# Kernel optimization log

Hardware: AMD Instinct MI355X
Metric: run time of the kernel (lower is better)

## Reference

```python
import jax, jax.numpy as jnp
import numpy as np

# PGA G(3,0,1) basis order: [1, e0, e1, e2, e3, e01, e02, e03, e12, e13, e23, e012, e013, e023, e123, e0123].
# The invariant inner product <rev(x) y>_0 only involves blades NOT containing e0; for those blades
# the metric contribution is +1, so it is a plain dot product over these 8 components.
_IP_IDX = np.array([0, 2, 3, 4, 8, 9, 10, 14])
_EPS = 1e-3  # config.normalizer_eps


def _normalizer(x):
    # _lin_square_normalizer: x / (x^2 + eps), a bounded ~1/x-style transform
    return x / (x * x + _EPS)


def setup_inputs() -> dict:
    key = jax.random.key(0)
    ks = jax.random.split(key, 7)
    B, H, N, CMV, CS = 2, 8, 2048, 16, 32
    f = lambda k, s: jax.random.normal(k, s, dtype=jnp.float32)
    return {
        "q_mv": f(ks[0], (B, H, N, CMV, 16)),
        "k_mv": f(ks[1], (B, H, N, CMV, 16)),
        "v_mv": f(ks[2], (B, H, N, CMV, 16)),
        "q_s": f(ks[3], (B, H, N, CS)),
        "k_s": f(ks[4], (B, H, N, CS)),
        "v_s": f(ks[5], (B, H, N, CS)),
        "log_weights": 0.1 * f(ks[6], (H, 1, CMV)),
    }


def reference(q_mv, k_mv, v_mv, q_s, k_s, v_s, log_weights):
    B, H, N, CMV, _ = q_mv.shape
    CS = q_s.shape[-1]

    # per-head, per-mv-channel learned positive weights, broadcast over items and blades
    w = jnp.exp(log_weights)[None, :, :, :, None]  # (1, H, 1, CMV, 1)

    # Term 1: weighted PGA inner product of multivector q/k (8 non-degenerate blades per channel)
    q_ip = (q_mv[..., _IP_IDX] * w).reshape(B, H, N, CMV * 8)
    k_ip = k_mv[..., _IP_IDX].reshape(B, H, N, CMV * 8)

    # Term 2: transformed scalar inner product <phi(q_s), psi(k_s)> with phi=psi=normalizer
    # Term 3: Euclidean scalar inner product <q_s, k_s>
    q_feat = jnp.concatenate([q_ip, _normalizer(q_s), q_s], axis=-1)  # (B,H,N, 8*CMV + 2*CS)
    k_feat = jnp.concatenate([k_ip, _normalizer(k_s), k_s], axis=-1)

    scale = 1.0 / jnp.sqrt(jnp.asarray(q_feat.shape[-1], dtype=q_feat.dtype))
    scores = jnp.einsum("bhid,bhjd->bhij", q_feat, k_feat) * scale  # (B,H,N,N)
    attn = jax.nn.softmax(scores, axis=-1)

    # Shared attention weights applied to flattened multivector + scalar values
    v_flat = jnp.concatenate([v_mv.reshape(B, H, N, CMV * 16), v_s], axis=-1)  # (B,H,N, 16*CMV+CS)
    out = jnp.einsum("bhij,bhjd->bhid", attn, v_flat)

    out_mv = out[..., : CMV * 16].reshape(B, H, N, CMV, 16)
    out_s = out[..., CMV * 16 :]
    return out_mv, out_s
```

## Files before the change

### kernel.cpp

```cpp
#include <hip/hip_runtime.h>

typedef float f32x4 __attribute__((ext_vector_type(4)));
typedef _Float16 f16x8 __attribute__((ext_vector_type(8)));
typedef _Float16 f16x4 __attribute__((ext_vector_type(4)));

#define NSEQ 2048
#define KVBLK 64
#define NITER (NSEQ / KVBLK)
#define KFBYTES (KVBLK * 384)
#define VTBYTES (288 * 2 * KVBLK)
#define TILEB (KFBYTES + VTBYTES)
#define KFOFF 0
#define VTOFF KFBYTES
#define PSTRIDE 72
#define WS_NEED (16ull * NITER * TILEB)

#define SCALE_L2E 0.10411754f
#define DEFER_THR 11.0f

__device__ __forceinline__ void async_copy16(const void* g, void* l) {
    __builtin_amdgcn_global_load_lds((const __attribute__((address_space(1))) unsigned int*)g,
                                     (__attribute__((address_space(3))) unsigned int*)l, 16, 0, 0);
}

__global__ __launch_bounds__(256)
void prep_kf(const float* __restrict__ k_mv, const float* __restrict__ k_s,
             unsigned char* __restrict__ ws)
{
    constexpr int IPIDX[8] = {0, 2, 3, 4, 8, 9, 10, 14};
    const int head = blockIdx.x >> 5, kt = blockIdx.x & 31;
    unsigned char* tb = ws + (size_t)(head * NITER + kt) * TILEB + KFOFF;
    const int tid = threadIdx.x;
    #pragma unroll
    for (int rep = 0; rep < 6; ++rep) {
        const int t = rep * 256 + tid;
        const int j = t & 63, oct = t >> 6;
        const size_t row = (size_t)head * NSEQ + kt * KVBLK + j;
        float v[8];
        if (oct < 16) {
            const float* p = k_mv + (row * 16 + oct) * 16;
            #pragma unroll
            for (int i = 0; i < 8; ++i) v[i] = p[IPIDX[i]];
        } else if (oct < 20) {
            const f32x4* p4 = (const f32x4*)(k_s + row * 32 + (oct - 16) * 8);
            f32x4 a = p4[0], b = p4[1];
            #pragma unroll
            for (int i = 0; i < 8; ++i) {
                float x = (i < 4) ? a[i & 3] : b[i & 3];
                v[i] = x / (x * x + 1e-3f);
            }
        } else {
            const f32x4* p4 = (const f32x4*)(k_s + row * 32 + (oct - 20) * 8);
            f32x4 a = p4[0], b = p4[1];
            #pragma unroll
            for (int i = 0; i < 8; ++i) v[i] = (i < 4) ? a[i & 3] : b[i & 3];
        }
        f16x8 o;
        #pragma unroll
        for (int i = 0; i < 8; ++i) o[i] = (_Float16)v[i];
        *(f16x8*)(tb + ((j * 384 + oct * 16) ^ ((j & 7) << 4))) = o;
    }
}

__global__ __launch_bounds__(256)
void prep_vt(const float* __restrict__ v_mv, const float* __restrict__ v_s,
             unsigned char* __restrict__ ws)
{
    const int head = blockIdx.x >> 5, kt = blockIdx.x & 31;
    unsigned char* tb = ws + (size_t)(head * NITER + kt) * TILEB + VTOFF;
    const int tid = threadIdx.x;
    const size_t row0 = (size_t)head * NSEQ + kt * KVBLK;
    {
        const int d = tid;
        float val[KVBLK];
        #pragma unroll
        for (int j = 0; j < KVBLK; ++j) val[j] = v_mv[(row0 + j) * 256 + d];
        #pragma unroll
        for (int jg = 0; jg < 8; ++jg) {
            f16x8 o;
            #pragma unroll
            for (int i = 0; i < 8; ++i) o[i] = (_Float16)val[jg * 8 + i];
            *(f16x8*)(tb + ((d * 128 + jg * 16) ^ ((d & 7) << 4))) = o;
        }
    }
    if (tid < 32) {
        const int d = 256 + tid;
        float val[KVBLK];
        #pragma unroll
        for (int j = 0; j < KVBLK; ++j) val[j] = v_s[(row0 + j) * 32 + tid];
        #pragma unroll
        for (int jg = 0; jg < 8; ++jg) {
            f16x8 o;
            #pragma unroll
            for (int i = 0; i < 8; ++i) o[i] = (_Float16)val[jg * 8 + i];
            *(f16x8*)(tb + ((d * 128 + jg * 16) ^ ((d & 7) << 4))) = o;
        }
    }
}

__global__ __launch_bounds__(512, 2)
void geoattn_main(const float* __restrict__ q_mv, const float* __restrict__ q_s,
                  const float* __restrict__ logw, const unsigned char* __restrict__ ws,
                  float* __restrict__ out)
{
    constexpr int IPIDX[8] = {0, 2, 3, 4, 8, 9, 10, 14};
    __shared__ __align__(16) unsigned char lbuf[2][TILEB];
    __shared__ __align__(16) _Float16 P_lds[128 * PSTRIDE];
    __shared__ __align__(16) float a_lds[128];

    const int bid  = blockIdx.x;
    const int head = (bid & 7) | ((bid >> 7) << 3);
    const int qt   = (bid >> 3) & 15;
    const int h    = head & 7;

    const int tid  = threadIdx.x;
    const int w    = tid >> 6;
    const int lane = tid & 63;
    const int lr   = lane & 15;
    const int lg   = lane >> 4;
    const int pr   = (w >> 1) * 32;
    const int e    = w & 1;

    const size_t rowbase = (size_t)head * NSEQ;
    const int q0 = qt * 128;
    const unsigned char* wsh = ws + (size_t)head * NITER * TILEB;

    #pragma unroll
    for (int c = 0; c < 8; ++c) {
        const int off = c * 8192 + tid * 16;
        if (off < TILEB) async_copy16(wsh + off, &lbuf[0][off]);
    }

    f16x8 qf[6];
    {
        const int qrow = q0 + w * 16 + lr;
        const float* qmv = q_mv + (rowbase + qrow) * 256;
        const float* qs  = q_s  + (rowbase + qrow) * 32;
        #pragma unroll
        for (int c = 0; c < 4; ++c) {
            const int cmv = 4 * c + lg;
            const float wgt = __expf(logw[h * 16 + cmv]) * SCALE_L2E;
            const float* p = qmv + cmv * 16;
            #pragma unroll
            for (int i = 0; i < 8; ++i)
                qf[c][i] = (_Float16)(p[IPIDX[i]] * wgt);
        }
        const f32x4* p4 = (const f32x4*)(qs + lg * 8);
        f32x4 a = p4[0], b = p4[1];
        #pragma unroll
        for (int i = 0; i < 8; ++i) {
            float x = (i < 4) ? a[i & 3] : b[i & 3];
            qf[4][i] = (_Float16)(SCALE_L2E * x / (x * x + 1e-3f));
            qf[5][i] = (_Float16)(SCALE_L2E * x);
        }
    }

    f32x4 acc[2][9];
    #pragma unroll
    for (int rg = 0; rg < 2; ++rg)
        #pragma unroll
        for (int dt = 0; dt < 9; ++dt) acc[rg][dt] = f32x4{0.f, 0.f, 0.f, 0.f};
    float mrun = -1e30f, lrun = 0.f;

    int cur = 0;
    for (int kt = 0; kt < NITER; ++kt) {
        if (kt < NITER - 1) {
            const unsigned char* src = wsh + (size_t)(kt + 1) * TILEB;
            #pragma unroll
            for (int c = 0; c < 8; ++c) {
                const int off = c * 8192 + tid * 16;
                if (off < TILEB) async_copy16(src + off, &lbuf[cur ^ 1][off]);
            }
            asm volatile("s_waitcnt vmcnt(7)" ::: "memory");
        } else {
            asm volatile("s_waitcnt vmcnt(0)" ::: "memory");
        }
        __builtin_amdgcn_s_barrier();
        asm volatile("" ::: "memory");

        const unsigned char* kb = lbuf[cur];

        f32x4 sacc[4];
        #pragma unroll
        for (int jt = 0; jt < 4; ++jt) sacc[jt] = f32x4{0.f, 0.f, 0.f, 0.f};
        #pragma unroll
        for (int jt = 0; jt < 4; ++jt) {
            const int j = jt * 16 + lr;
            #pragma unroll
            for (int c = 0; c < 6; ++c) {
                f16x8 kf = *(const f16x8*)(kb + KFOFF +
                            ((j * 384 + c * 64 + lg * 16) ^ ((lr & 7) << 4)));
                sacc[jt] = __builtin_amdgcn_mfma_f32_16x16x32_f16(kf, qf[c], sacc[jt], 0, 0, 0);
            }
        }

        float mloc;
        {
            float t0 = fmaxf(fmaxf(sacc[0][0], sacc[0][1]), fmaxf(sacc[0][2], sacc[0][3]));
            #pragma unroll
            for (int jt = 1; jt < 4; ++jt) {
                float t1 = fmaxf(fmaxf(sacc[jt][0], sacc[jt][1]), fmaxf(sacc[jt][2], sacc[jt][3]));
                t0 = fmaxf(t0, t1);
            }
            t0 = fmaxf(t0, __shfl_xor(t0, 16));
            t0 = fmaxf(t0, __shfl_xor(t0, 32));
            mloc = t0;
        }
        const bool need = (mloc > mrun + DEFER_THR);
        const float mnew = need ? mloc : mrun;
        const float alpha = exp2f(mrun - mnew);
        mrun = mnew;
        if (lg == 0) a_lds[w * 16 + lr] = alpha;

        float ps = 0.f;
        f16x4 pk[4];
        #pragma unroll
        for (int jt = 0; jt < 4; ++jt)
            #pragma unroll
            for (int r = 0; r < 4; ++r) {
                const float p = exp2f(sacc[jt][r] - mrun);
                ps += p;
                pk[jt][r] = (_Float16)p;
            }
        ps += __shfl_xor(ps, 16);
        ps += __shfl_xor(ps, 32);
        lrun = lrun * alpha + ps;
        #pragma unroll
        for (int jt = 0; jt < 4; ++jt)
            *(f16x4*)(&P_lds[(w * 16 + lr) * PSTRIDE + jt * 16 + lg * 4]) = pk[jt];

        asm volatile("s_waitcnt lgkmcnt(0)" ::: "memory");
        __builtin_amdgcn_s_barrier();
        asm volatile("" ::: "memory");

        f32x4 al[2];
        al[0] = *(const f32x4*)&a_lds[pr + lg * 4];
        al[1] = *(const f32x4*)&a_lds[pr + 16 + lg * 4];
        const bool rs = (al[0][0] < 1.f) || (al[0][1] < 1.f) || (al[0][2] < 1.f) || (al[0][3] < 1.f) ||
                        (al[1][0] < 1.f) || (al[1][1] < 1.f) || (al[1][2] < 1.f) || (al[1][3] < 1.f);
        if (__ballot(rs)) {
            #pragma unroll
            for (int rg = 0; rg < 2; ++rg)
                #pragma unroll
                for (int dt = 0; dt < 9; ++dt)
                    #pragma unroll
                    for (int r = 0; r < 4; ++r) acc[rg][dt][r] *= al[rg][r];
        }

        #pragma unroll
        for (int kc = 0; kc < 2; ++kc) {
            f16x8 pf0 = *(const f16x8*)(&P_lds[(pr + lr) * PSTRIDE + kc * 32 + lg * 8]);
            f16x8 pf1 = *(const f16x8*)(&P_lds[(pr + 16 + lr) * PSTRIDE + kc * 32 + lg * 8]);
            #pragma unroll
            for (int dt = 0; dt < 9; ++dt) {
                const int d = e * 144 + dt * 16 + lr;
                f16x8 vf = *(const f16x8*)(kb + VTOFF +
                            ((d * 128 + kc * 64 + lg * 16) ^ ((lr & 7) << 4)));
                acc[0][dt] = __builtin_amdgcn_mfma_f32_16x16x32_f16(pf0, vf, acc[0][dt], 0, 0, 0);
                acc[1][dt] = __builtin_amdgcn_mfma_f32_16x16x32_f16(pf1, vf, acc[1][dt], 0, 0, 0);
            }
        }

        asm volatile("" ::: "memory");
        __builtin_amdgcn_s_barrier();
        cur ^= 1;
    }

    if (lg == 0) a_lds[w * 16 + lr] = lrun;
    asm volatile("s_waitcnt lgkmcnt(0)" ::: "memory");
    __builtin_amdgcn_s_barrier();
    f32x4 lv[2];
    lv[0] = *(const f32x4*)&a_lds[pr + lg * 4];
    lv[1] = *(const f32x4*)&a_lds[pr + 16 + lg * 4];
    #pragma unroll
    for (int rg = 0; rg < 2; ++rg) {
        #pragma unroll
        for (int r = 0; r < 4; ++r) {
            const float inv = 1.0f / lv[rg][r];
            const int row = q0 + pr + rg * 16 + lg * 4 + r;
            float* omv = out + (rowbase + row) * 256;
            float* os  = out + 8388608ull + (rowbase + row) * 32;
            #pragma unroll
            for (int dt = 0; dt < 9; ++dt) {
                const int d = e * 144 + dt * 16 + lr;
                const float val = acc[rg][dt][r] * inv;
                if (d < 256) omv[d] = val;
                else         os[d - 256] = val;
            }
        }
    }
}

#define FKSTRIDE 200
#define FVSTRIDE 72
__global__ __launch_bounds__(256, 2)
void geoattn_fallback(const float* __restrict__ q_mv, const float* __restrict__ k_mv,
                      const float* __restrict__ v_mv, const float* __restrict__ q_s,
                      const float* __restrict__ k_s, const float* __restrict__ v_s,
                      const float* __restrict__ logw, float* __restrict__ out)
{
    constexpr int IPIDX[8] = {0, 2, 3, 4, 8, 9, 10, 14};
    __shared__ __align__(16) _Float16 lds_k[64 * FKSTRIDE];
    __shared__ __align__(16) _Float16 lds_vt[288 * FVSTRIDE];
    __shared__ __align__(16) _Float16 lds_p[4 * 16 * FVSTRIDE];

    const int bid  = blockIdx.x;
    const int head = (bid & 7) | ((bid >> 8) << 3);
    const int qt   = (bid >> 3) & 31;
    const int h    = head & 7;
    const int tid  = threadIdx.x;
    const int w    = tid >> 6;
    const int lane = tid & 63;
    const int lr   = lane & 15;
    const int lg   = lane >> 4;
    const size_t rowbase = (size_t)head * NSEQ;
    const int q0 = qt * 64;
    const float scale = 0.07216878364870323f;

    f16x8 qf[6];
    {
        const int qrow = q0 + w * 16 + lr;
        const float* qmv = q_mv + (rowbase + qrow) * 256;
        const float* qs  = q_s  + (rowbase + qrow) * 32;
        #pragma unroll
        for (int c = 0; c < 4; ++c) {
            const int cmv = 4 * c + lg;
            const float wgt = __expf(logw[h * 16 + cmv]) * scale;
            const float* p = qmv + cmv * 16;
            #pragma unroll
            for (int i = 0; i < 8; ++i) qf[c][i] = (_Float16)(p[IPIDX[i]] * wgt);
        }
        const f32x4* p4 = (const f32x4*)(qs + lg * 8);
        f32x4 a = p4[0], b = p4[1];
        #pragma unroll
        for (int i = 0; i < 8; ++i) {
            float x = (i < 4) ? a[i & 3] : b[i & 3];
            qf[4][i] = (_Float16)(scale * x / (x * x + 1e-3f));
            qf[5][i] = (_Float16)(scale * x);
        }
    }
    f32x4 acc[18];
    #pragma unroll
    for (int dt = 0; dt < 18; ++dt) acc[dt] = f32x4{0.f, 0.f, 0.f, 0.f};
    float mrun[4] = {-1e30f, -1e30f, -1e30f, -1e30f};
    float lrun[4] = {0.f, 0.f, 0.f, 0.f};

    for (int kt = 0; kt < 32; ++kt) {
        const int j0 = kt * 64;
        __syncthreads();
        #pragma unroll
        for (int rep = 0; rep < 6; ++rep) {
            const int t = rep * 256 + tid;
            const int j = t & 63, oct = t >> 6;
            const size_t krow = rowbase + j0 + j;
            float v[8];
            if (oct < 16) {
                const float* p = k_mv + (krow * 16 + oct) * 16;
                #pragma unroll
                for (int i = 0; i < 8; ++i) v[i] = p[IPIDX[i]];
            } else if (oct < 20) {
                const f32x4* p4 = (const f32x4*)(k_s + krow * 32 + (oct - 16) * 8);
                f32x4 a = p4[0], b = p4[1];
                #pragma unroll
                for (int i = 0; i < 8; ++i) {
                    float x = (i < 4) ? a[i & 3] : b[i & 3];
                    v[i] = x / (x * x + 1e-3f);
                }
            } else {
                const f32x4* p4 = (const f32x4*)(k_s + krow * 32 + (oct - 20) * 8);
                f32x4 a = p4[0], b = p4[1];
                #pragma unroll
                for (int i = 0; i < 8; ++i) v[i] = (i < 4) ? a[i & 3] : b[i & 3];
            }
            f16x8 o;
            #pragma unroll
            for (int i = 0; i < 8; ++i) o[i] = (_Float16)v[i];
            *(f16x8*)(&lds_k[j * FKSTRIDE + oct * 8]) = o;
        }
        #pragma unroll
        for (int rep = 0; rep < 9; ++rep) {
            const int t = rep * 256 + tid;
            const int j = t & 63, oct = t >> 6;
            const size_t vrow = rowbase + j0 + j;
            const float* src = (oct < 32) ? (v_mv + vrow * 256 + oct * 8)
                                          : (v_s  + vrow * 32 + (oct - 32) * 8);
            const f32x4* p4 = (const f32x4*)src;
            f32x4 a = p4[0], b = p4[1];
            const int d0 = oct * 8;
            #pragma unroll
            for (int i = 0; i < 8; ++i)
                lds_vt[(d0 + i) * FVSTRIDE + j] = (_Float16)((i < 4) ? a[i & 3] : b[i & 3]);
        }
        __syncthreads();
        f32x4 sacc[4];
        #pragma unroll
        for (int nt = 0; nt < 4; ++nt) {
            sacc[nt] = f32x4{0.f, 0.f, 0.f, 0.f};
            #pragma unroll
            for (int c = 0; c < 6; ++c) {
                f16x8 kf = *(const f16x8*)(&lds_k[(lr + 16 * nt) * FKSTRIDE + 32 * c + lg * 8]);
                sacc[nt] = __builtin_amdgcn_mfma_f32_16x16x32_f16(qf[c], kf, sacc[nt], 0, 0, 0);
            }
        }
        float tmax[4], alpha[4];
        #pragma unroll
        for (int r = 0; r < 4; ++r) {
            float t0 = fmaxf(fmaxf(sacc[0][r], sacc[1][r]), fmaxf(sacc[2][r], sacc[3][r]));
            #pragma unroll
            for (int mm = 1; mm < 16; mm <<= 1) t0 = fmaxf(t0, __shfl_xor(t0, mm));
            tmax[r] = t0;
        }
        bool need = false;
        #pragma unroll
        for (int r = 0; r < 4; ++r) {
            float mnew = fmaxf(mrun[r], tmax[r]);
            need = need || (tmax[r] > mrun[r]);
            alpha[r] = __expf(mrun[r] - mnew);
            mrun[r] = mnew;
        }
        float pvv[4][4];
        float psum[4] = {0.f, 0.f, 0.f, 0.f};
        #pragma unroll
        for (int nt = 0; nt < 4; ++nt)
            #pragma unroll
            for (int r = 0; r < 4; ++r) {
                float p = __expf(sacc[nt][r] - mrun[r]);
                pvv[nt][r] = p;
                psum[r] += p;
            }
        #pragma unroll
        for (int r = 0; r < 4; ++r) {
            float s = psum[r];
            #pragma unroll
            for (int mm = 1; mm < 16; mm <<= 1) s += __shfl_xor(s, mm);
            lrun[r] = lrun[r] * alpha[r] + s;
        }
        if (__ballot(need)) {
            #pragma unroll
            for (int dt = 0; dt < 18; ++dt)
                #pragma unroll
                for (int r = 0; r < 4; ++r) acc[dt][r] *= alpha[r];
        }
        _Float16* pbf = &lds_p[w * 16 * FVSTRIDE];
        #pragma unroll
        for (int nt = 0; nt < 4; ++nt)
            #pragma unroll
            for (int r = 0; r < 4; ++r)
                pbf[(lg * 4 + r) * FVSTRIDE + lr + 16 * nt] = (_Float16)pvv[nt][r];
        #pragma unroll
        for (int ch = 0; ch < 2; ++ch) {
            f16x8 pf = *(const f16x8*)(&pbf[lr * FVSTRIDE + 32 * ch + lg * 8]);
            #pragma unroll
            for (int dt = 0; dt < 18; ++dt) {
                f16x8 vf = *(const f16x8*)(&lds_vt[(lr + 16 * dt) * FVSTRIDE + 32 * ch + lg * 8]);
                acc[dt] = __builtin_amdgcn_mfma_f32_16x16x32_f16(pf, vf, acc[dt], 0, 0, 0);
            }
        }
    }
    const int orow = q0 + w * 16 + lg * 4;
    #pragma unroll
    for (int r = 0; r < 4; ++r) {
        const float inv = 1.0f / lrun[r];
        float* omv = out + (rowbase + orow + r) * 256;
        float* os  = out + 8388608ull + (rowbase + orow + r) * 32;
        #pragma unroll
        for (int dt = 0; dt < 18; ++dt) {
            const int d = lr + 16 * dt;
            const float val = acc[dt][r] * inv;
            if (d < 256) omv[d] = val;
            else         os[d - 256] = val;
        }
    }
}

extern "C" void kernel_launch(void* const* d_in, const int* in_sizes, int n_in,
                              void* d_out, int out_size, void* d_ws, size_t ws_size,
                              hipStream_t stream) {
    (void)in_sizes; (void)n_in; (void)out_size;
    const float* q_mv = (const float*)d_in[0];
    const float* k_mv = (const float*)d_in[1];
    const float* v_mv = (const float*)d_in[2];
    const float* q_s  = (const float*)d_in[3];
    const float* k_s  = (const float*)d_in[4];
    const float* v_s  = (const float*)d_in[5];
    const float* logw = (const float*)d_in[6];
    float* out = (float*)d_out;

    if (ws_size >= WS_NEED) {
        unsigned char* ws = (unsigned char*)d_ws;
        prep_kf<<<dim3(512), dim3(256), 0, stream>>>(k_mv, k_s, ws);
        prep_vt<<<dim3(512), dim3(256), 0, stream>>>(v_mv, v_s, ws);
        geoattn_main<<<dim3(256), dim3(512), 0, stream>>>(q_mv, q_s, logw, ws, out);
    } else {
        geoattn_fallback<<<dim3(512), dim3(256), 0, stream>>>(q_mv, k_mv, v_mv, q_s, k_s, v_s, logw, out);
    }
}
```

Measured before the change: 125.3 us.

## Halve KV and query tiles, double grid, simplify prefetch sync, add setprio

Shrinks the KV block from 64 to 32 keys and the query tile from 128 to 64 rows. Blocks now have 256 threads instead of 512 and the grid doubles, so more workgroups are in flight for latency hiding. The loop now waits for the current tile and syncs before issuing the next tile's prefetch, which removes the trailing barrier. The MFMA sections are wrapped in s_setprio. In exchange there are twice as many iterations with barrier and softmax overhead per key, and each loaded tile is reused across fewer query rows.

```diff
diff --git a/kernel.cpp b/kernel.cpp
--- a/kernel.cpp
+++ b/kernel.cpp
@@ -5,14 +5,14 @@
 typedef _Float16 f16x4 __attribute__((ext_vector_type(4)));
 
 #define NSEQ 2048
-#define KVBLK 64
+#define KVBLK 32
 #define NITER (NSEQ / KVBLK)
 #define KFBYTES (KVBLK * 384)
 #define VTBYTES (288 * 2 * KVBLK)
-#define TILEB (KFBYTES + VTBYTES)
+#define TILEB 32768
 #define KFOFF 0
 #define VTOFF KFBYTES
-#define PSTRIDE 72
+#define PSTRIDE 40
 #define WS_NEED (16ull * NITER * TILEB)
 
 #define SCALE_L2E 0.10411754f
@@ -28,13 +28,13 @@
              unsigned char* __restrict__ ws)
 {
     constexpr int IPIDX[8] = {0, 2, 3, 4, 8, 9, 10, 14};
-    const int head = blockIdx.x >> 5, kt = blockIdx.x & 31;
+    const int head = blockIdx.x >> 6, kt = blockIdx.x & 63;
     unsigned char* tb = ws + (size_t)(head * NITER + kt) * TILEB + KFOFF;
     const int tid = threadIdx.x;
     #pragma unroll
-    for (int rep = 0; rep < 6; ++rep) {
+    for (int rep = 0; rep < 3; ++rep) {
         const int t = rep * 256 + tid;
-        const int j = t & 63, oct = t >> 6;
+        const int j = t & 31, oct = t >> 5;
         const size_t row = (size_t)head * NSEQ + kt * KVBLK + j;
         float v[8];
         if (oct < 16) {
@@ -66,7 +66,7 @@
 void prep_vt(const float* __restrict__ v_mv, const float* __restrict__ v_s,
              unsigned char* __restrict__ ws)
 {
-    const int head = blockIdx.x >> 5, kt = blockIdx.x & 31;
+    const int head = blockIdx.x >> 6, kt = blockIdx.x & 63;
     unsigned char* tb = ws + (size_t)(head * NITER + kt) * TILEB + VTOFF;
     const int tid = threadIdx.x;
     const size_t row0 = (size_t)head * NSEQ + kt * KVBLK;
@@ -76,11 +76,11 @@
         #pragma unroll
         for (int j = 0; j < KVBLK; ++j) val[j] = v_mv[(row0 + j) * 256 + d];
         #pragma unroll
-        for (int jg = 0; jg < 8; ++jg) {
+        for (int jg = 0; jg < 4; ++jg) {
             f16x8 o;
             #pragma unroll
             for (int i = 0; i < 8; ++i) o[i] = (_Float16)val[jg * 8 + i];
-            *(f16x8*)(tb + ((d * 128 + jg * 16) ^ ((d & 7) << 4))) = o;
+            *(f16x8*)(tb + ((d * 64 + jg * 16) ^ ((d & 7) << 4))) = o;
         }
     }
     if (tid < 32) {
@@ -89,28 +89,28 @@
         #pragma unroll
         for (int j = 0; j < KVBLK; ++j) val[j] = v_s[(row0 + j) * 32 + tid];
         #pragma unroll
-        for (int jg = 0; jg < 8; ++jg) {
+        for (int jg = 0; jg < 4; ++jg) {
             f16x8 o;
             #pragma unroll
             for (int i = 0; i < 8; ++i) o[i] = (_Float16)val[jg * 8 + i];
-            *(f16x8*)(tb + ((d * 128 + jg * 16) ^ ((d & 7) << 4))) = o;
-        }
-    }
-}
-
-__global__ __launch_bounds__(512, 2)
+            *(f16x8*)(tb + ((d * 64 + jg * 16) ^ ((d & 7) << 4))) = o;
+        }
+    }
+}
+
+__global__ __launch_bounds__(256, 2)
 void geoattn_main(const float* __restrict__ q_mv, const float* __restrict__ q_s,
                   const float* __restrict__ logw, const unsigned char* __restrict__ ws,
                   float* __restrict__ out)
 {
     constexpr int IPIDX[8] = {0, 2, 3, 4, 8, 9, 10, 14};
     __shared__ __align__(16) unsigned char lbuf[2][TILEB];
-    __shared__ __align__(16) _Float16 P_lds[128 * PSTRIDE];
-    __shared__ __align__(16) float a_lds[128];
+    __shared__ __align__(16) _Float16 P_lds[64 * PSTRIDE];
+    __shared__ __align__(16) float a_lds[64];
 
     const int bid  = blockIdx.x;
-    const int head = (bid & 7) | ((bid >> 7) << 3);
-    const int qt   = (bid >> 3) & 15;
+    const int head = (bid & 7) | ((bid >> 8) << 3);
+    const int qt   = (bid >> 3) & 31;
     const int h    = head & 7;
 
     const int tid  = threadIdx.x;
@@ -122,14 +122,12 @@
     const int e    = w & 1;
 
     const size_t rowbase = (size_t)head * NSEQ;
-    const int q0 = qt * 128;
+    const int q0 = qt * 64;
     const unsigned char* wsh = ws + (size_t)head * NITER * TILEB;
 
     #pragma unroll
-    for (int c = 0; c < 8; ++c) {
-        const int off = c * 8192 + tid * 16;
-        if (off < TILEB) async_copy16(wsh + off, &lbuf[0][off]);
-    }
+    for (int c = 0; c < 8; ++c)
+        async_copy16(wsh + c * 4096 + tid * 16, &lbuf[0][c * 4096 + tid * 16]);
 
     f16x8 qf[6];
     {
@@ -164,27 +162,24 @@
 
     int cur = 0;
     for (int kt = 0; kt < NITER; ++kt) {
+        asm volatile("s_waitcnt vmcnt(0)" ::: "memory");
+        __builtin_amdgcn_s_barrier();
+        asm volatile("" ::: "memory");
         if (kt < NITER - 1) {
             const unsigned char* src = wsh + (size_t)(kt + 1) * TILEB;
             #pragma unroll
-            for (int c = 0; c < 8; ++c) {
-                const int off = c * 8192 + tid * 16;
-                if (off < TILEB) async_copy16(src + off, &lbuf[cur ^ 1][off]);
-            }
-            asm volatile("s_waitcnt vmcnt(7)" ::: "memory");
-        } else {
-            asm volatile("s_waitcnt vmcnt(0)" ::: "memory");
-        }
-        __builtin_amdgcn_s_barrier();
-        asm volatile("" ::: "memory");
+            for (int c = 0; c < 8; ++c)
+                async_copy16(src + c * 4096 + tid * 16, &lbuf[cur ^ 1][c * 4096 + tid * 16]);
+        }
 
         const unsigned char* kb = lbuf[cur];
 
-        f32x4 sacc[4];
-        #pragma unroll
-        for (int jt = 0; jt < 4; ++jt) sacc[jt] = f32x4{0.f, 0.f, 0.f, 0.f};
-        #pragma unroll
-        for (int jt = 0; jt < 4; ++jt) {
+        f32x4 sacc[2];
+        sacc[0] = f32x4{0.f, 0.f, 0.f, 0.f};
+        sacc[1] = f32x4{0.f, 0.f, 0.f, 0.f};
+        __builtin_amdgcn_s_setprio(1);
+        #pragma unroll
+        for (int jt = 0; jt < 2; ++jt) {
             const int j = jt * 16 + lr;
             #pragma unroll
             for (int c = 0; c < 6; ++c) {
@@ -193,15 +188,13 @@
                 sacc[jt] = __builtin_amdgcn_mfma_f32_16x16x32_f16(kf, qf[c], sacc[jt], 0, 0, 0);
             }
         }
+        __builtin_amdgcn_s_setprio(0);
 
         float mloc;
         {
             float t0 = fmaxf(fmaxf(sacc[0][0], sacc[0][1]), fmaxf(sacc[0][2], sacc[0][3]));
-            #pragma unroll
-            for (int jt = 1; jt < 4; ++jt) {
-                float t1 = fmaxf(fmaxf(sacc[jt][0], sacc[jt][1]), fmaxf(sacc[jt][2], sacc[jt][3]));
-                t0 = fmaxf(t0, t1);
-            }
+            float t1 = fmaxf(fmaxf(sacc[1][0], sacc[1][1]), fmaxf(sacc[1][2], sacc[1][3]));
+            t0 = fmaxf(t0, t1);
             t0 = fmaxf(t0, __shfl_xor(t0, 16));
             t0 = fmaxf(t0, __shfl_xor(t0, 32));
             mloc = t0;
@@ -213,9 +206,9 @@
         if (lg == 0) a_lds[w * 16 + lr] = alpha;
 
         float ps = 0.f;
-        f16x4 pk[4];
-        #pragma unroll
-        for (int jt = 0; jt < 4; ++jt)
+        f16x4 pk[2];
+        #pragma unroll
+        for (int jt = 0; jt < 2; ++jt)
             #pragma unroll
             for (int r = 0; r < 4; ++r) {
                 const float p = exp2f(sacc[jt][r] - mrun);
@@ -226,7 +219,7 @@
         ps += __shfl_xor(ps, 32);
         lrun = lrun * alpha + ps;
         #pragma unroll
-        for (int jt = 0; jt < 4; ++jt)
+        for (int jt = 0; jt < 2; ++jt)
             *(f16x4*)(&P_lds[(w * 16 + lr) * PSTRIDE + jt * 16 + lg * 4]) = pk[jt];
 
         asm volatile("s_waitcnt lgkmcnt(0)" ::: "memory");
@@ -247,25 +240,23 @@
                     for (int r = 0; r < 4; ++r) acc[rg][dt][r] *= al[rg][r];
         }
 
-        #pragma unroll
-        for (int kc = 0; kc < 2; ++kc) {
-            f16x8 pf0 = *(const f16x8*)(&P_lds[(pr + lr) * PSTRIDE + kc * 32 + lg * 8]);
-            f16x8 pf1 = *(const f16x8*)(&P_lds[(pr + 16 + lr) * PSTRIDE + kc * 32 + lg * 8]);
-            #pragma unroll
-            for (int dt = 0; dt < 9; ++dt) {
-                const int d = e * 144 + dt * 16 + lr;
-                f16x8 vf = *(const f16x8*)(kb + VTOFF +
-                            ((d * 128 + kc * 64 + lg * 16) ^ ((lr & 7) << 4)));
-                acc[0][dt] = __builtin_amdgcn_mfma_f32_16x16x32_f16(pf0, vf, acc[0][dt], 0, 0, 0);
-                acc[1][dt] = __builtin_amdgcn_mfma_f32_16x16x32_f16(pf1, vf, acc[1][dt], 0, 0, 0);
-            }
-        }
-
-        asm volatile("" ::: "memory");
-        __builtin_amdgcn_s_barrier();
+        f16x8 pf0 = *(const f16x8*)(&P_lds[(pr + lr) * PSTRIDE + lg * 8]);
+        f16x8 pf1 = *(const f16x8*)(&P_lds[(pr + 16 + lr) * PSTRIDE + lg * 8]);
+        __builtin_amdgcn_s_setprio(1);
+        #pragma unroll
+        for (int dt = 0; dt < 9; ++dt) {
+            const int d = e * 144 + dt * 16 + lr;
+            f16x8 vf = *(const f16x8*)(kb + VTOFF +
+                        ((d * 64 + lg * 16) ^ ((lr & 7) << 4)));
+            acc[0][dt] = __builtin_amdgcn_mfma_f32_16x16x32_f16(pf0, vf, acc[0][dt], 0, 0, 0);
+            acc[1][dt] = __builtin_amdgcn_mfma_f32_16x16x32_f16(pf1, vf, acc[1][dt], 0, 0, 0);
+        }
+        __builtin_amdgcn_s_setprio(0);
+
         cur ^= 1;
     }
 
+    __builtin_amdgcn_s_barrier();
     if (lg == 0) a_lds[w * 16 + lr] = lrun;
     asm volatile("s_waitcnt lgkmcnt(0)" ::: "memory");
     __builtin_amdgcn_s_barrier();
@@ -488,9 +479,9 @@
 
     if (ws_size >= WS_NEED) {
         unsigned char* ws = (unsigned char*)d_ws;
-        prep_kf<<<dim3(512), dim3(256), 0, stream>>>(k_mv, k_s, ws);
-        prep_vt<<<dim3(512), dim3(256), 0, stream>>>(v_mv, v_s, ws);
-        geoattn_main<<<dim3(256), dim3(512), 0, stream>>>(q_mv, q_s, logw, ws, out);
+        prep_kf<<<dim3(1024), dim3(256), 0, stream>>>(k_mv, k_s, ws);
+        prep_vt<<<dim3(1024), dim3(256), 0, stream>>>(v_mv, v_s, ws);
+        geoattn_main<<<dim3(512), dim3(256), 0, stream>>>(q_mv, q_s, logw, ws, out);
     } else {
         geoattn_fallback<<<dim3(512), dim3(256), 0, stream>>>(q_mv, k_mv, v_mv, q_s, k_s, v_s, logw, out);
     }
```

New measurement: 134.2 us. +7.1%, slower.

## Make each wave own its query rows end-to-end, dropping cross-wave P/alpha exchange

Applied to the files above, without the earlier changes.

Before this change, pairs of waves shared P and alpha through LDS: each wave computed scores for 16 rows, then did PV for 32 rows over half of the output dims. Now each wave keeps its own 16 rows through all 288 output dims, with a private P buffer and alpha broadcast by shuffles. This removes the mid-iteration barrier and the a_lds round trip, leaving one barrier per tile. It also adds s_setprio around the MFMA sections and moves the wait to the start of the loop. In exchange each wave reads every V fragment itself, roughly doubling LDS reads of V per wave, and the wait at the top of the iteration is now a full vmcnt(0).

```diff
diff --git a/kernel.cpp b/kernel.cpp
--- a/kernel.cpp
+++ b/kernel.cpp
@@ -105,8 +105,7 @@
 {
     constexpr int IPIDX[8] = {0, 2, 3, 4, 8, 9, 10, 14};
     __shared__ __align__(16) unsigned char lbuf[2][TILEB];
-    __shared__ __align__(16) _Float16 P_lds[128 * PSTRIDE];
-    __shared__ __align__(16) float a_lds[128];
+    __shared__ __align__(16) _Float16 P_all[8][16 * PSTRIDE];
 
     const int bid  = blockIdx.x;
     const int head = (bid & 7) | ((bid >> 7) << 3);
@@ -118,8 +117,6 @@
     const int lane = tid & 63;
     const int lr   = lane & 15;
     const int lg   = lane >> 4;
-    const int pr   = (w >> 1) * 32;
-    const int e    = w & 1;
 
     const size_t rowbase = (size_t)head * NSEQ;
     const int q0 = qt * 128;
@@ -155,15 +152,18 @@
         }
     }
 
-    f32x4 acc[2][9];
-    #pragma unroll
-    for (int rg = 0; rg < 2; ++rg)
-        #pragma unroll
-        for (int dt = 0; dt < 9; ++dt) acc[rg][dt] = f32x4{0.f, 0.f, 0.f, 0.f};
+    f32x4 acc[18];
+    #pragma unroll
+    for (int dt = 0; dt < 18; ++dt) acc[dt] = f32x4{0.f, 0.f, 0.f, 0.f};
     float mrun = -1e30f, lrun = 0.f;
+
+    _Float16* pb = &P_all[w][0];
 
     int cur = 0;
     for (int kt = 0; kt < NITER; ++kt) {
+        asm volatile("s_waitcnt vmcnt(0)" ::: "memory");
+        __builtin_amdgcn_s_barrier();
+        asm volatile("" ::: "memory");
         if (kt < NITER - 1) {
             const unsigned char* src = wsh + (size_t)(kt + 1) * TILEB;
             #pragma unroll
@@ -171,18 +171,14 @@
                 const int off = c * 8192 + tid * 16;
                 if (off < TILEB) async_copy16(src + off, &lbuf[cur ^ 1][off]);
             }
-            asm volatile("s_waitcnt vmcnt(7)" ::: "memory");
-        } else {
-            asm volatile("s_waitcnt vmcnt(0)" ::: "memory");
-        }
-        __builtin_amdgcn_s_barrier();
-        asm volatile("" ::: "memory");
+        }
 
         const unsigned char* kb = lbuf[cur];
 
         f32x4 sacc[4];
         #pragma unroll
         for (int jt = 0; jt < 4; ++jt) sacc[jt] = f32x4{0.f, 0.f, 0.f, 0.f};
+        __builtin_amdgcn_s_setprio(1);
         #pragma unroll
         for (int jt = 0; jt < 4; ++jt) {
             const int j = jt * 16 + lr;
@@ -193,6 +189,7 @@
                 sacc[jt] = __builtin_amdgcn_mfma_f32_16x16x32_f16(kf, qf[c], sacc[jt], 0, 0, 0);
             }
         }
+        __builtin_amdgcn_s_setprio(0);
 
         float mloc;
         {
@@ -210,83 +207,62 @@
         const float mnew = need ? mloc : mrun;
         const float alpha = exp2f(mrun - mnew);
         mrun = mnew;
-        if (lg == 0) a_lds[w * 16 + lr] = alpha;
-
+        if (__ballot(need)) {
+            float ar[4];
+            #pragma unroll
+            for (int r = 0; r < 4; ++r) ar[r] = __shfl(alpha, lg * 4 + r, 16);
+            #pragma unroll
+            for (int dt = 0; dt < 18; ++dt)
+                #pragma unroll
+                for (int r = 0; r < 4; ++r) acc[dt][r] *= ar[r];
+            lrun *= alpha;
+        }
         float ps = 0.f;
-        f16x4 pk[4];
-        #pragma unroll
-        for (int jt = 0; jt < 4; ++jt)
+        #pragma unroll
+        for (int jt = 0; jt < 4; ++jt) {
+            f16x4 pk;
             #pragma unroll
             for (int r = 0; r < 4; ++r) {
                 const float p = exp2f(sacc[jt][r] - mrun);
                 ps += p;
-                pk[jt][r] = (_Float16)p;
-            }
+                pk[r] = (_Float16)p;
+            }
+            *(f16x4*)(&pb[lr * PSTRIDE + jt * 16 + lg * 4]) = pk;
+        }
         ps += __shfl_xor(ps, 16);
         ps += __shfl_xor(ps, 32);
-        lrun = lrun * alpha + ps;
-        #pragma unroll
-        for (int jt = 0; jt < 4; ++jt)
-            *(f16x4*)(&P_lds[(w * 16 + lr) * PSTRIDE + jt * 16 + lg * 4]) = pk[jt];
-
-        asm volatile("s_waitcnt lgkmcnt(0)" ::: "memory");
-        __builtin_amdgcn_s_barrier();
-        asm volatile("" ::: "memory");
-
-        f32x4 al[2];
-        al[0] = *(const f32x4*)&a_lds[pr + lg * 4];
-        al[1] = *(const f32x4*)&a_lds[pr + 16 + lg * 4];
-        const bool rs = (al[0][0] < 1.f) || (al[0][1] < 1.f) || (al[0][2] < 1.f) || (al[0][3] < 1.f) ||
-                        (al[1][0] < 1.f) || (al[1][1] < 1.f) || (al[1][2] < 1.f) || (al[1][3] < 1.f);
-        if (__ballot(rs)) {
-            #pragma unroll
-            for (int rg = 0; rg < 2; ++rg)
-                #pragma unroll
-                for (int dt = 0; dt < 9; ++dt)
-                    #pragma unroll
-                    for (int r = 0; r < 4; ++r) acc[rg][dt][r] *= al[rg][r];
-        }
-
-        #pragma unroll
-        for (int kc = 0; kc < 2; ++kc) {
-            f16x8 pf0 = *(const f16x8*)(&P_lds[(pr + lr) * PSTRIDE + kc * 32 + lg * 8]);
-            f16x8 pf1 = *(const f16x8*)(&P_lds[(pr + 16 + lr) * PSTRIDE + kc * 32 + lg * 8]);
-            #pragma unroll
-            for (int dt = 0; dt < 9; ++dt) {
-                const int d = e * 144 + dt * 16 + lr;
-                f16x8 vf = *(const f16x8*)(kb + VTOFF +
-                            ((d * 128 + kc * 64 + lg * 16) ^ ((lr & 7) << 4)));
-                acc[0][dt] = __builtin_amdgcn_mfma_f32_16x16x32_f16(pf0, vf, acc[0][dt], 0, 0, 0);
-                acc[1][dt] = __builtin_amdgcn_mfma_f32_16x16x32_f16(pf1, vf, acc[1][dt], 0, 0, 0);
-            }
-        }
-
-        asm volatile("" ::: "memory");
-        __builtin_amdgcn_s_barrier();
+        lrun += ps;
+
+        f16x8 pf0 = *(const f16x8*)(&pb[lr * PSTRIDE + lg * 8]);
+        f16x8 pf1 = *(const f16x8*)(&pb[lr * PSTRIDE + 32 + lg * 8]);
+        __builtin_amdgcn_s_setprio(1);
+        #pragma unroll
+        for (int dt = 0; dt < 18; ++dt) {
+            const int d = dt * 16 + lr;
+            const int vb = VTOFF + d * 128 + lg * 16;
+            f16x8 vf0 = *(const f16x8*)(kb + ((vb) ^ ((d & 7) << 4)));
+            f16x8 vf1 = *(const f16x8*)(kb + ((vb + 64) ^ ((d & 7) << 4)));
+            acc[dt] = __builtin_amdgcn_mfma_f32_16x16x32_f16(pf0, vf0, acc[dt], 0, 0, 0);
+            acc[dt] = __builtin_amdgcn_mfma_f32_16x16x32_f16(pf1, vf1, acc[dt], 0, 0, 0);
+        }
+        __builtin_amdgcn_s_setprio(0);
+
         cur ^= 1;
     }
 
-    if (lg == 0) a_lds[w * 16 + lr] = lrun;
-    asm volatile("s_waitcnt lgkmcnt(0)" ::: "memory");
-    __builtin_amdgcn_s_barrier();
-    f32x4 lv[2];
-    lv[0] = *(const f32x4*)&a_lds[pr + lg * 4];
-    lv[1] = *(const f32x4*)&a_lds[pr + 16 + lg * 4];
-    #pragma unroll
-    for (int rg = 0; rg < 2; ++rg) {
-        #pragma unroll
-        for (int r = 0; r < 4; ++r) {
-            const float inv = 1.0f / lv[rg][r];
-            const int row = q0 + pr + rg * 16 + lg * 4 + r;
-            float* omv = out + (rowbase + row) * 256;
-            float* os  = out + 8388608ull + (rowbase + row) * 32;
-            #pragma unroll
-            for (int dt = 0; dt < 9; ++dt) {
-                const int d = e * 144 + dt * 16 + lr;
-                const float val = acc[rg][dt][r] * inv;
-                if (d < 256) omv[d] = val;
-                else         os[d - 256] = val;
-            }
+    #pragma unroll
+    for (int r = 0; r < 4; ++r) {
+        const float lv = __shfl(lrun, lg * 4 + r, 16);
+        const float inv = 1.0f / lv;
+        const int row = q0 + w * 16 + lg * 4 + r;
+        float* omv = out + (rowbase + row) * 256;
+        float* os  = out + 8388608ull + (rowbase + row) * 32;
+        #pragma unroll
+        for (int dt = 0; dt < 18; ++dt) {
+            const int d = dt * 16 + lr;
+            const float val = acc[dt][r] * inv;
+            if (d < 256) omv[d] = val;
+            else         os[d - 256] = val;
         }
     }
 }
```

After: 128.6 us. 2.6% more time.

## Software-pipeline PV matmul one tile behind QK with double-buffered P

Applied to the files above, without the earlier changes.

Restructures the main loop so each iteration first runs the P·V MFMA for the previous KV tile, then issues the next tile's prefetch and computes QK scores and softmax for the current tile. P and the alpha rescale buffers are double-buffered in LDS, a final epilogue handles the last tile, and s_setprio wraps the MFMA sections. The aim is to cut a barrier per iteration and let the softmax of one tile overlap with the matmul of another across waves. In exchange, the prefetch is now issued later and waited on with vmcnt(0) at the top of each iteration, which shortens the window for hiding load latency. LDS use also grows by about 18KB.

```diff
diff --git a/kernel.cpp b/kernel.cpp
--- a/kernel.cpp
+++ b/kernel.cpp
@@ -105,8 +105,8 @@
 {
     constexpr int IPIDX[8] = {0, 2, 3, 4, 8, 9, 10, 14};
     __shared__ __align__(16) unsigned char lbuf[2][TILEB];
-    __shared__ __align__(16) _Float16 P_lds[128 * PSTRIDE];
-    __shared__ __align__(16) float a_lds[128];
+    __shared__ __align__(16) _Float16 P2[2][128 * PSTRIDE];
+    __shared__ __align__(16) float a2[2][128];
 
     const int bid  = blockIdx.x;
     const int head = (bid & 7) | ((bid >> 7) << 3);
@@ -164,6 +164,48 @@
 
     int cur = 0;
     for (int kt = 0; kt < NITER; ++kt) {
+        asm volatile("s_waitcnt vmcnt(0) lgkmcnt(0)" ::: "memory");
+        __builtin_amdgcn_s_barrier();
+        asm volatile("" ::: "memory");
+
+        if (kt > 0) {
+            const int pbuf = (kt - 1) & 1;
+            f32x4 al[2];
+            al[0] = *(const f32x4*)&a2[pbuf][pr + lg * 4];
+            al[1] = *(const f32x4*)&a2[pbuf][pr + 16 + lg * 4];
+            const bool rs = (al[0][0] < 1.f) || (al[0][1] < 1.f) || (al[0][2] < 1.f) || (al[0][3] < 1.f) ||
+                            (al[1][0] < 1.f) || (al[1][1] < 1.f) || (al[1][2] < 1.f) || (al[1][3] < 1.f);
+            if (__ballot(rs)) {
+                #pragma unroll
+                for (int rg = 0; rg < 2; ++rg)
+                    #pragma unroll
+                    for (int dt = 0; dt < 9; ++dt)
+                        #pragma unroll
+                        for (int r = 0; r < 4; ++r) acc[rg][dt][r] *= al[rg][r];
+            }
+            const _Float16* pbr = &P2[pbuf][0];
+            const unsigned char* vb = lbuf[cur ^ 1];
+            __builtin_amdgcn_s_setprio(1);
+            #pragma unroll
+            for (int kc = 0; kc < 2; ++kc) {
+                f16x8 pf0 = *(const f16x8*)(&pbr[(pr + lr) * PSTRIDE + kc * 32 + lg * 8]);
+                f16x8 pf1 = *(const f16x8*)(&pbr[(pr + 16 + lr) * PSTRIDE + kc * 32 + lg * 8]);
+                #pragma unroll
+                for (int dt = 0; dt < 9; ++dt) {
+                    const int d = e * 144 + dt * 16 + lr;
+                    f16x8 vf = *(const f16x8*)(vb + VTOFF +
+                                ((d * 128 + kc * 64 + lg * 16) ^ ((lr & 7) << 4)));
+                    acc[0][dt] = __builtin_amdgcn_mfma_f32_16x16x32_f16(pf0, vf, acc[0][dt], 0, 0, 0);
+                    acc[1][dt] = __builtin_amdgcn_mfma_f32_16x16x32_f16(pf1, vf, acc[1][dt], 0, 0, 0);
+                }
+            }
+            __builtin_amdgcn_s_setprio(0);
+        }
+
+        asm volatile("s_waitcnt lgkmcnt(0)" ::: "memory");
+        __builtin_amdgcn_s_barrier();
+        asm volatile("" ::: "memory");
+
         if (kt < NITER - 1) {
             const unsigned char* src = wsh + (size_t)(kt + 1) * TILEB;
             #pragma unroll
@@ -171,18 +213,14 @@
                 const int off = c * 8192 + tid * 16;
                 if (off < TILEB) async_copy16(src + off, &lbuf[cur ^ 1][off]);
             }
-            asm volatile("s_waitcnt vmcnt(7)" ::: "memory");
-        } else {
-            asm volatile("s_waitcnt vmcnt(0)" ::: "memory");
-        }
-        __builtin_amdgcn_s_barrier();
-        asm volatile("" ::: "memory");
+        }
 
         const unsigned char* kb = lbuf[cur];
 
         f32x4 sacc[4];
         #pragma unroll
         for (int jt = 0; jt < 4; ++jt) sacc[jt] = f32x4{0.f, 0.f, 0.f, 0.f};
+        __builtin_amdgcn_s_setprio(1);
         #pragma unroll
         for (int jt = 0; jt < 4; ++jt) {
             const int j = jt * 16 + lr;
@@ -193,6 +231,7 @@
                 sacc[jt] = __builtin_amdgcn_mfma_f32_16x16x32_f16(kf, qf[c], sacc[jt], 0, 0, 0);
             }
         }
+        __builtin_amdgcn_s_setprio(0);
 
         float mloc;
         {
@@ -210,32 +249,36 @@
         const float mnew = need ? mloc : mrun;
         const float alpha = exp2f(mrun - mnew);
         mrun = mnew;
-        if (lg == 0) a_lds[w * 16 + lr] = alpha;
+        if (lg == 0) a2[kt & 1][w * 16 + lr] = alpha;
 
         float ps = 0.f;
-        f16x4 pk[4];
-        #pragma unroll
-        for (int jt = 0; jt < 4; ++jt)
+        _Float16* pbw = &P2[kt & 1][0];
+        #pragma unroll
+        for (int jt = 0; jt < 4; ++jt) {
+            f16x4 pk;
             #pragma unroll
             for (int r = 0; r < 4; ++r) {
                 const float p = exp2f(sacc[jt][r] - mrun);
                 ps += p;
-                pk[jt][r] = (_Float16)p;
-            }
+                pk[r] = (_Float16)p;
+            }
+            *(f16x4*)(&pbw[(w * 16 + lr) * PSTRIDE + jt * 16 + lg * 4]) = pk;
+        }
         ps += __shfl_xor(ps, 16);
         ps += __shfl_xor(ps, 32);
         lrun = lrun * alpha + ps;
-        #pragma unroll
-        for (int jt = 0; jt < 4; ++jt)
-            *(f16x4*)(&P_lds[(w * 16 + lr) * PSTRIDE + jt * 16 + lg * 4]) = pk[jt];
-
-        asm volatile("s_waitcnt lgkmcnt(0)" ::: "memory");
-        __builtin_amdgcn_s_barrier();
-        asm volatile("" ::: "memory");
-
+
+        cur ^= 1;
+    }
+
+    asm volatile("s_waitcnt lgkmcnt(0)" ::: "memory");
+    __builtin_amdgcn_s_barrier();
+    asm volatile("" ::: "memory");
+    {
+        const int pbuf = (NITER - 1) & 1;
         f32x4 al[2];
-        al[0] = *(const f32x4*)&a_lds[pr + lg * 4];
-        al[1] = *(const f32x4*)&a_lds[pr + 16 + lg * 4];
+        al[0] = *(const f32x4*)&a2[pbuf][pr + lg * 4];
+        al[1] = *(const f32x4*)&a2[pbuf][pr + 16 + lg * 4];
         const bool rs = (al[0][0] < 1.f) || (al[0][1] < 1.f) || (al[0][2] < 1.f) || (al[0][3] < 1.f) ||
                         (al[1][0] < 1.f) || (al[1][1] < 1.f) || (al[1][2] < 1.f) || (al[1][3] < 1.f);
         if (__ballot(rs)) {
@@ -246,32 +289,30 @@
                     #pragma unroll
                     for (int r = 0; r < 4; ++r) acc[rg][dt][r] *= al[rg][r];
         }
-
+        const _Float16* pbr = &P2[pbuf][0];
+        const unsigned char* vb = lbuf[cur ^ 1];
         #pragma unroll
         for (int kc = 0; kc < 2; ++kc) {
-            f16x8 pf0 = *(const f16x8*)(&P_lds[(pr + lr) * PSTRIDE + kc * 32 + lg * 8]);
-            f16x8 pf1 = *(const f16x8*)(&P_lds[(pr + 16 + lr) * PSTRIDE + kc * 32 + lg * 8]);
+            f16x8 pf0 = *(const f16x8*)(&pbr[(pr + lr) * PSTRIDE + kc * 32 + lg * 8]);
+            f16x8 pf1 = *(const f16x8*)(&pbr[(pr + 16 + lr) * PSTRIDE + kc * 32 + lg * 8]);
             #pragma unroll
             for (int dt = 0; dt < 9; ++dt) {
                 const int d = e * 144 + dt * 16 + lr;
-                f16x8 vf = *(const f16x8*)(kb + VTOFF +
+                f16x8 vf = *(const f16x8*)(vb + VTOFF +
                             ((d * 128 + kc * 64 + lg * 16) ^ ((lr & 7) << 4)));
                 acc[0][dt] = __builtin_amdgcn_mfma_f32_16x16x32_f16(pf0, vf, acc[0][dt], 0, 0, 0);
                 acc[1][dt] = __builtin_amdgcn_mfma_f32_16x16x32_f16(pf1, vf, acc[1][dt], 0, 0, 0);
             }
         }
-
-        asm volatile("" ::: "memory");
-        __builtin_amdgcn_s_barrier();
-        cur ^= 1;
-    }
-
-    if (lg == 0) a_lds[w * 16 + lr] = lrun;
+    }
+
+    __builtin_amdgcn_s_barrier();
+    if (lg == 0) a2[0][w * 16 + lr] = lrun;
     asm volatile("s_waitcnt lgkmcnt(0)" ::: "memory");
     __builtin_amdgcn_s_barrier();
     f32x4 lv[2];
-    lv[0] = *(const f32x4*)&a_lds[pr + lg * 4];
-    lv[1] = *(const f32x4*)&a_lds[pr + 16 + lg * 4];
+    lv[0] = *(const f32x4*)&a2[0][pr + lg * 4];
+    lv[1] = *(const f32x4*)&a2[0][pr + 16 + lg * 4];
     #pragma unroll
     for (int rg = 0; rg < 2; ++rg) {
         #pragma unroll
```

Result: slower. 128.1 us (+2.2%).
